# Kernel optimization log

Measured on AMD Instinct MI355X. Metric: run time of the kernel, lower is better.

The kernel has to match this reference:

```python
import jax, jax.numpy as jnp
import numpy as np

NUM_CLASSES = 150
FEAT_DIM = 128
N = 1_000_000
TEMPERATURE = 0.15
EPS = 1e-12


def _l2_normalize(x, axis=-1):
    # matches F.normalize(p=2): x / max(||x||, eps)
    n = jnp.sqrt(jnp.sum(x * x, axis=axis, keepdims=True))
    return x / jnp.maximum(n, EPS)


def setup_inputs() -> dict:
    key = jax.random.key(0)
    k1, k2, k3 = jax.random.split(key, 3)
    features = jax.random.normal(k1, (N, FEAT_DIM), dtype=jnp.float32)
    labels = jax.random.randint(k2, (N,), 0, NUM_CLASSES, dtype=jnp.int64)
    # prototypes buffer: random normal, L2-normalized per class (as in _initialize_prototypes)
    prototypes = _l2_normalize(jax.random.normal(k3, (NUM_CLASSES, FEAT_DIM), dtype=jnp.float32))
    return {"features": features, "labels": labels, "prototypes": prototypes}


def reference(features, labels, prototypes):
    # proto_contrastive_loss: normalize, similarity logits, per-sample CE, mean
    f = _l2_normalize(features)                      # [N, D]
    logits = (f @ prototypes.T) / TEMPERATURE        # [N, C]
    logz = jax.nn.logsumexp(logits, axis=-1)         # [N]
    picked = jnp.take_along_axis(logits, labels[:, None].astype(jnp.int32), axis=-1)[:, 0]
    losses = logz - picked                           # cross_entropy, reduction='none'
    return jnp.mean(losses)
```

## Files before the change

### kernel.cpp

```cpp
#include <hip/hip_runtime.h>


#define NS 1000000
#define NC 150
#define NCP 160
#define FD 128
#define NTILE (NS / 16)
#define NBLK 1024
#define NWAVE (NBLK * 4)

static constexpr float INV_T  = 1.0f / 0.15f;
static constexpr float MB     = 1.0f / 0.15f;
static constexpr float LOG2E  = 1.4426950408889634f;
static constexpr float B2     = -MB * LOG2E;

typedef __attribute__((ext_vector_type(8))) short short8;
typedef __attribute__((ext_vector_type(4))) float f32x4;

__device__ __forceinline__ short f2bf(float x) {
    unsigned u = __builtin_bit_cast(unsigned, x);
    unsigned r = (u + 0x7fffu + ((u >> 16) & 1u)) >> 16;
    return (short)r;
}

__global__ __launch_bounds__(256) void proto_prep(
    const float* __restrict__ protos, unsigned short* __restrict__ dst)
{
    const int tid = threadIdx.x;
#pragma unroll 4
    for (int i = 0; i < (NCP * FD) / 256; ++i) {
        int idx = i * 256 + tid;
        int row = idx >> 7;
        int col = idx & 127;
        float v = (row < NC) ? protos[row * FD + col] : 0.0f;
        dst[idx] = (unsigned short)f2bf(v);
    }
}

__global__ __launch_bounds__(256) void proto_ce_mfma(
    const float*          __restrict__ feats,
    const int*            __restrict__ labels,
    const unsigned short* __restrict__ protos_bf,
    double*               __restrict__ partials)
{
    __shared__ __align__(16) char lds[NCP * FD * 2];

    const int tid = threadIdx.x;

    {
        const uint4* src = (const uint4*)protos_bf;
#pragma unroll
        for (int i = 0; i < (NCP * FD * 2) / 16 / 256; ++i) {
            int e8  = i * 256 + tid;
            int row = e8 >> 4;
            int binr = (e8 & 15) << 4;
            int dst = row * 256 + (binr ^ ((row & 7) << 4));
            *(uint4*)(lds + dst) = src[e8];
        }
    }
    __syncthreads();

    const int lane = tid & 63;
    const int wave = tid >> 6;
    const int col  = lane & 15;
    const int grp  = lane >> 4;
    const int gw   = blockIdx.x * 4 + wave;

    const int sw  = (col & 7) << 4;
    const int a0  = col * 256 + ((grp * 16) ^ (sw & 0x30));
    const int ahi = sw & 0x40;

    const int lrel = -grp * 4;
    const int vcnt = 6 - grp * 4;

    const long lane_off = (long)col * (FD / 4) + grp * 2;

    float loss_acc = 0.0f;

    for (int t = gw; t < NTILE; t += NWAVE) {
        const float4* fp = (const float4*)(feats + (long)t * (16 * FD)) + lane_off;
        float4 buf[8];
#pragma unroll
        for (int kb = 0; kb < 4; ++kb) {
            buf[kb * 2]     = fp[kb * 8];
            buf[kb * 2 + 1] = fp[kb * 8 + 1];
        }
        const int lbl = labels[t * 16 + col];

        float ssq = 0.0f;
#pragma unroll
        for (int i = 0; i < 8; ++i)
            ssq += buf[i].x * buf[i].x + buf[i].y * buf[i].y +
                   buf[i].z * buf[i].z + buf[i].w * buf[i].w;
        ssq += __shfl_xor(ssq, 16, 64);
        ssq += __shfl_xor(ssq, 32, 64);
        const float scl = rsqrtf(fmaxf(ssq, 1e-24f));

        f32x4 acc[10];
#pragma unroll
        for (int i = 0; i < 10; ++i) acc[i] = (f32x4){0.f, 0.f, 0.f, 0.f};

#pragma unroll
        for (int kb = 0; kb < 4; ++kb) {
            float4 A = buf[kb * 2], Bv = buf[kb * 2 + 1];
            short8 bfr;
            bfr[0] = f2bf(A.x);  bfr[1] = f2bf(A.y);
            bfr[2] = f2bf(A.z);  bfr[3] = f2bf(A.w);
            bfr[4] = f2bf(Bv.x); bfr[5] = f2bf(Bv.y);
            bfr[6] = f2bf(Bv.z); bfr[7] = f2bf(Bv.w);

            const char* ap = lds + (a0 + ((kb * 64) ^ ahi));
#pragma unroll
            for (int tt = 0; tt < 10; ++tt) {
                short8 af = *(const short8*)(ap + tt * 4096);
                acc[tt] = __builtin_amdgcn_mfma_f32_16x16x32_bf16(af, bfr, acc[tt], 0, 0, 0);
            }
        }

        const float k2 = scl * (INV_T * LOG2E);
        const int   lm = lbl + lrel;
        float s0 = 0.f, s1 = 0.f, s2 = 0.f, s3 = 0.f;
        float pick = 0.0f;
#pragma unroll
        for (int tt = 0; tt < 10; ++tt) {
#pragma unroll
            for (int r = 0; r < 4; ++r) {
                float a = acc[tt][r];
                float e = exp2f(fmaf(a, k2, B2));
                if (tt < 9) {
                    if      (r == 0) s0 += e;
                    else if (r == 1) s1 += e;
                    else if (r == 2) s2 += e;
                    else             s3 += e;
                } else {
                    s0 += (r < vcnt) ? e : 0.0f;
                }
                pick = (tt * 16 + r == lm) ? a : pick;
            }
        }
        float ssum = (s0 + s1) + (s2 + s3);
        ssum += __shfl_xor(ssum, 16, 64);
        ssum += __shfl_xor(ssum, 32, 64);
        pick += __shfl_xor(pick, 16, 64);
        pick += __shfl_xor(pick, 32, 64);

        loss_acc += __logf(ssum) + MB - pick * (scl * INV_T);
    }

    loss_acc += __shfl_xor(loss_acc, 1, 64);
    loss_acc += __shfl_xor(loss_acc, 2, 64);
    loss_acc += __shfl_xor(loss_acc, 4, 64);
    loss_acc += __shfl_xor(loss_acc, 8, 64);
    if (lane == 0)
        atomicAdd(&partials[gw & 255], (double)loss_acc);
}

__global__ __launch_bounds__(256) void proto_ce_final(
    const double* __restrict__ partials, float* __restrict__ out)
{
    const int tid = threadIdx.x;
    double v = partials[tid];
#pragma unroll
    for (int off = 32; off > 0; off >>= 1)
        v += __shfl_down(v, off, 64);
    __shared__ double w[4];
    if ((tid & 63) == 0) w[tid >> 6] = v;
    __syncthreads();
    if (tid == 0)
        out[0] = (float)((w[0] + w[1] + w[2] + w[3]) * (1.0 / (double)NS));
}

extern "C" void kernel_launch(void* const* d_in, const int* in_sizes, int n_in,
                              void* d_out, int out_size, void* d_ws, size_t ws_size,
                              hipStream_t stream)
{
    const float* feats  = (const float*)d_in[0];
    const int*   labels = (const int*)d_in[1];
    const float* protos = (const float*)d_in[2];

    unsigned short* protos_bf = (unsigned short*)d_ws;
    double* partials = (double*)((char*)d_ws + NCP * FD * 2);

    (void)hipMemsetAsync(partials, 0, 256 * sizeof(double), stream);
    proto_prep<<<1, 256, 0, stream>>>(protos, protos_bf);
    proto_ce_mfma<<<NBLK, 256, 0, stream>>>(feats, labels, protos_bf, partials);
    proto_ce_final<<<1, 256, 0, stream>>>(partials, (float*)d_out);
}
```

Measured before the change: 188.7 us.

## Use one-tile-per-block grid with direct global-to-LDS loads for features and prototypes

Replaces the persistent grid-stride loop with a grid of NS/64 blocks, each processing one 16-row tile per wave. Features and pre-swizzled bf16 prototypes are copied straight into LDS with global_load_lds, with an XOR swizzle to avoid bank conflicts. The prep kernel now writes prototypes in the swizzled layout so the copy is linear. This trades register-held feature loads and cross-iteration latency hiding for many short-lived blocks that each reload the 40KB prototype table and use more LDS, which limits occupancy.

```diff
diff --git a/kernel.cpp b/kernel.cpp
--- a/kernel.cpp
+++ b/kernel.cpp
@@ -6,56 +6,72 @@
 #define NCP 160
 #define FD 128
 #define NTILE (NS / 16)
-#define NBLK 1024
-#define NWAVE (NBLK * 4)
 
-static constexpr float INV_T  = 1.0f / 0.15f;
-static constexpr float MB     = 1.0f / 0.15f;
-static constexpr float LOG2E  = 1.4426950408889634f;
-static constexpr float B2     = -MB * LOG2E;
+static constexpr float INV_T = 1.0f / 0.15f;
+static constexpr float MB    = 1.0f / 0.15f;
+static constexpr float LOG2E = 1.4426950408889634f;
+static constexpr float B2    = -MB * LOG2E;
 
 typedef __attribute__((ext_vector_type(8))) short short8;
 typedef __attribute__((ext_vector_type(4))) float f32x4;
+typedef unsigned int u32;
 
-__device__ __forceinline__ short f2bf(float x) {
+#define GLOAD_LDS16(g, l) \
+    __builtin_amdgcn_global_load_lds((const __attribute__((address_space(1))) u32*)(g), \
+                                     (__attribute__((address_space(3))) u32*)(l), 16, 0, 0)
+
+__device__ __forceinline__ unsigned f2bf_u(float x) {
     unsigned u = __builtin_bit_cast(unsigned, x);
-    unsigned r = (u + 0x7fffu + ((u >> 16) & 1u)) >> 16;
-    return (short)r;
+    return (u + 0x7fffu + ((u >> 16) & 1u)) >> 16;
 }
 
 __global__ __launch_bounds__(256) void proto_prep(
-    const float* __restrict__ protos, unsigned short* __restrict__ dst)
+    const float* __restrict__ protos, u32* __restrict__ dst)
 {
     const int tid = threadIdx.x;
-#pragma unroll 4
-    for (int i = 0; i < (NCP * FD) / 256; ++i) {
-        int idx = i * 256 + tid;
-        int row = idx >> 7;
-        int col = idx & 127;
-        float v = (row < NC) ? protos[row * FD + col] : 0.0f;
-        dst[idx] = (unsigned short)f2bf(v);
+#pragma unroll
+    for (int i = 0; i < 10; ++i) {
+        int c  = i * 256 + tid;
+        int r  = c >> 4;
+        int cb = c & 15;
+        float f[8];
+#pragma unroll
+        for (int j = 0; j < 8; ++j)
+            f[j] = (r < NC) ? protos[r * FD + cb * 8 + j] : 0.0f;
+        u32 w[4];
+#pragma unroll
+        for (int j = 0; j < 4; ++j)
+            w[j] = f2bf_u(f[2 * j]) | (f2bf_u(f[2 * j + 1]) << 16);
+        u32* out = dst + (r * 64 + ((cb ^ (r & 7)) << 2));
+        out[0] = w[0]; out[1] = w[1]; out[2] = w[2]; out[3] = w[3];
     }
 }
 
 __global__ __launch_bounds__(256) void proto_ce_mfma(
-    const float*          __restrict__ feats,
-    const int*            __restrict__ labels,
-    const unsigned short* __restrict__ protos_bf,
-    double*               __restrict__ partials)
+    const float* __restrict__ feats,
+    const int*   __restrict__ labels,
+    const u32*   __restrict__ protos_sw,
+    double*      __restrict__ partials)
 {
-    __shared__ __align__(16) char lds[NCP * FD * 2];
+    __shared__ __align__(16) char ldsA[NCP * FD * 2];
+    __shared__ __align__(16) char ldsF[64 * FD * 4];
 
     const int tid = threadIdx.x;
 
     {
-        const uint4* src = (const uint4*)protos_bf;
+        const char* ps = (const char*)protos_sw;
 #pragma unroll
-        for (int i = 0; i < (NCP * FD * 2) / 16 / 256; ++i) {
-            int e8  = i * 256 + tid;
-            int row = e8 >> 4;
-            int binr = (e8 & 15) << 4;
-            int dst = row * 256 + (binr ^ ((row & 7) << 4));
-            *(uint4*)(lds + dst) = src[e8];
+        for (int i = 0; i < 10; ++i) {
+            int c = i * 256 + tid;
+            GLOAD_LDS16(ps + c * 16, ldsA + c * 16);
+        }
+        const char* fs = (const char*)(feats + (long)blockIdx.x * (64 * FD));
+#pragma unroll
+        for (int i = 0; i < 8; ++i) {
+            int c = i * 256 + tid;
+            int r = c >> 5;
+            int x = c & 31;
+            GLOAD_LDS16(fs + r * 512 + ((x ^ (r & 7)) << 4), ldsF + c * 16);
         }
     }
     __syncthreads();
@@ -70,89 +86,81 @@
     const int a0  = col * 256 + ((grp * 16) ^ (sw & 0x30));
     const int ahi = sw & 0x40;
 
+    const int frow = (wave * 16 + col) * 512;
+    const int s3   = col & 7;
+    const char* f0 = ldsF + frow + (((grp << 1) ^ s3) << 4);
+    const char* f1 = ldsF + frow + ((((grp << 1) | 1) ^ s3) << 4);
+
     const int lrel = -grp * 4;
     const int vcnt = 6 - grp * 4;
 
-    const long lane_off = (long)col * (FD / 4) + grp * 2;
+    const int lbl = labels[gw * 16 + col];
 
-    float loss_acc = 0.0f;
+    f32x4 acc[10];
+#pragma unroll
+    for (int i = 0; i < 10; ++i) acc[i] = (f32x4){0.f, 0.f, 0.f, 0.f};
 
-    for (int t = gw; t < NTILE; t += NWAVE) {
-        const float4* fp = (const float4*)(feats + (long)t * (16 * FD)) + lane_off;
-        float4 buf[8];
+    float ssq = 0.0f;
 #pragma unroll
-        for (int kb = 0; kb < 4; ++kb) {
-            buf[kb * 2]     = fp[kb * 8];
-            buf[kb * 2 + 1] = fp[kb * 8 + 1];
-        }
-        const int lbl = labels[t * 16 + col];
+    for (int kb = 0; kb < 4; ++kb) {
+        float4 A = *(const float4*)(f0 + kb * 128);
+        float4 Bv = *(const float4*)(f1 + kb * 128);
+        ssq += A.x * A.x + A.y * A.y + A.z * A.z + A.w * A.w;
+        ssq += Bv.x * Bv.x + Bv.y * Bv.y + Bv.z * Bv.z + Bv.w * Bv.w;
 
-        float ssq = 0.0f;
-#pragma unroll
-        for (int i = 0; i < 8; ++i)
-            ssq += buf[i].x * buf[i].x + buf[i].y * buf[i].y +
-                   buf[i].z * buf[i].z + buf[i].w * buf[i].w;
-        ssq += __shfl_xor(ssq, 16, 64);
-        ssq += __shfl_xor(ssq, 32, 64);
-        const float scl = rsqrtf(fmaxf(ssq, 1e-24f));
+        short8 bfr;
+        bfr[0] = (short)f2bf_u(A.x);  bfr[1] = (short)f2bf_u(A.y);
+        bfr[2] = (short)f2bf_u(A.z);  bfr[3] = (short)f2bf_u(A.w);
+        bfr[4] = (short)f2bf_u(Bv.x); bfr[5] = (short)f2bf_u(Bv.y);
+        bfr[6] = (short)f2bf_u(Bv.z); bfr[7] = (short)f2bf_u(Bv.w);
 
-        f32x4 acc[10];
-#pragma unroll
-        for (int i = 0; i < 10; ++i) acc[i] = (f32x4){0.f, 0.f, 0.f, 0.f};
-
-#pragma unroll
-        for (int kb = 0; kb < 4; ++kb) {
-            float4 A = buf[kb * 2], Bv = buf[kb * 2 + 1];
-            short8 bfr;
-            bfr[0] = f2bf(A.x);  bfr[1] = f2bf(A.y);
-            bfr[2] = f2bf(A.z);  bfr[3] = f2bf(A.w);
-            bfr[4] = f2bf(Bv.x); bfr[5] = f2bf(Bv.y);
-            bfr[6] = f2bf(Bv.z); bfr[7] = f2bf(Bv.w);
-
-            const char* ap = lds + (a0 + ((kb * 64) ^ ahi));
-#pragma unroll
-            for (int tt = 0; tt < 10; ++tt) {
-                short8 af = *(const short8*)(ap + tt * 4096);
-                acc[tt] = __builtin_amdgcn_mfma_f32_16x16x32_bf16(af, bfr, acc[tt], 0, 0, 0);
-            }
-        }
-
-        const float k2 = scl * (INV_T * LOG2E);
-        const int   lm = lbl + lrel;
-        float s0 = 0.f, s1 = 0.f, s2 = 0.f, s3 = 0.f;
-        float pick = 0.0f;
+        const char* ap = ldsA + (a0 + ((kb * 64) ^ ahi));
 #pragma unroll
         for (int tt = 0; tt < 10; ++tt) {
-#pragma unroll
-            for (int r = 0; r < 4; ++r) {
-                float a = acc[tt][r];
-                float e = exp2f(fmaf(a, k2, B2));
-                if (tt < 9) {
-                    if      (r == 0) s0 += e;
-                    else if (r == 1) s1 += e;
-                    else if (r == 2) s2 += e;
-                    else             s3 += e;
-                } else {
-                    s0 += (r < vcnt) ? e : 0.0f;
-                }
-                pick = (tt * 16 + r == lm) ? a : pick;
-            }
+            short8 af = *(const short8*)(ap + tt * 4096);
+            acc[tt] = __builtin_amdgcn_mfma_f32_16x16x32_bf16(af, bfr, acc[tt], 0, 0, 0);
         }
-        float ssum = (s0 + s1) + (s2 + s3);
-        ssum += __shfl_xor(ssum, 16, 64);
-        ssum += __shfl_xor(ssum, 32, 64);
-        pick += __shfl_xor(pick, 16, 64);
-        pick += __shfl_xor(pick, 32, 64);
-
-        loss_acc += __logf(ssum) + MB - pick * (scl * INV_T);
     }
 
-    loss_acc += __shfl_xor(loss_acc, 1, 64);
-    loss_acc += __shfl_xor(loss_acc, 2, 64);
-    loss_acc += __shfl_xor(loss_acc, 4, 64);
-    loss_acc += __shfl_xor(loss_acc, 8, 64);
+    ssq += __shfl_xor(ssq, 16, 64);
+    ssq += __shfl_xor(ssq, 32, 64);
+    const float scl = rsqrtf(fmaxf(ssq, 1e-24f));
+
+    const float k2 = scl * (INV_T * LOG2E);
+    const int   lm = lbl + lrel;
+    float s0 = 0.f, s1 = 0.f, s2 = 0.f, s3v = 0.f;
+    float pick = 0.0f;
+#pragma unroll
+    for (int tt = 0; tt < 10; ++tt) {
+#pragma unroll
+        for (int r = 0; r < 4; ++r) {
+            float a = acc[tt][r];
+            float e = exp2f(fmaf(a, k2, B2));
+            if (tt < 9) {
+                if      (r == 0) s0 += e;
+                else if (r == 1) s1 += e;
+                else if (r == 2) s2 += e;
+                else             s3v += e;
+            } else {
+                s0 += (r < vcnt) ? e : 0.0f;
+            }
+            pick = (tt * 16 + r == lm) ? a : pick;
+        }
+    }
+    float ssum = (s0 + s1) + (s2 + s3v);
+    ssum += __shfl_xor(ssum, 16, 64);
+    ssum += __shfl_xor(ssum, 32, 64);
+    pick += __shfl_xor(pick, 16, 64);
+    pick += __shfl_xor(pick, 32, 64);
+
+    float loss = __logf(ssum) + MB - pick * (scl * INV_T);
+
+    loss += __shfl_xor(loss, 1, 64);
+    loss += __shfl_xor(loss, 2, 64);
+    loss += __shfl_xor(loss, 4, 64);
+    loss += __shfl_xor(loss, 8, 64);
     if (lane == 0)
-        atomicAdd(&partials[gw & 255], (double)loss_acc);
+        atomicAdd(&partials[gw & 255], (double)loss);
 }
 
 __global__ __launch_bounds__(256) void proto_ce_final(
@@ -178,11 +186,11 @@
     const int*   labels = (const int*)d_in[1];
     const float* protos = (const float*)d_in[2];
 
-    unsigned short* protos_bf = (unsigned short*)d_ws;
+    u32* protos_sw = (u32*)d_ws;
     double* partials = (double*)((char*)d_ws + NCP * FD * 2);
 
     (void)hipMemsetAsync(partials, 0, 256 * sizeof(double), stream);
-    proto_prep<<<1, 256, 0, stream>>>(protos, protos_bf);
-    proto_ce_mfma<<<NBLK, 256, 0, stream>>>(feats, labels, protos_bf, partials);
+    proto_prep<<<1, 256, 0, stream>>>(protos, protos_sw);
+    proto_ce_mfma<<<NS / 64, 256, 0, stream>>>(feats, labels, protos_sw, partials);
     proto_ce_final<<<1, 256, 0, stream>>>(partials, (float*)d_out);
 }
```

Result: faster. 167.9 us (-11.0%).
